# Optimization experiments

Measured on AMD Instinct MI355X. Metric: run time of the kernel, lower is better.

## Reference

```python
import jax, jax.numpy as jnp
import numpy as np

B, N, C_IN, C_OUT, H_MLP, STEPS, DEG = 8, 128, 512, 512, 128, 10, 16
E = B * N * DEG  # edges per side


def _seg_mean(v, idx, n):
    s = jax.ops.segment_sum(v, idx, num_segments=n)
    c = jax.ops.segment_sum(jnp.ones((v.shape[0], 1), v.dtype), idx, num_segments=n)
    return s / jnp.maximum(c, 1.0)


def _relconv(x, ei, W1, W2, Wr, br):
    n = x.shape[0]
    src, dst = ei[0], ei[1]
    out1 = _seg_mean((x @ W1)[src], dst, n)  # flow source_to_target, mean aggr
    out2 = _seg_mean((x @ W2)[dst], src, n)  # flow target_to_source, mean aggr
    return x @ Wr + br + out1 + out2


def _gnn(x, ei, p):
    # GNNForEmbedding: 1 RelConv layer, LayerNorm(relu(.)), cat=True, lin=True (eval: dropout off)
    W1, W2, Wr, br, g, b, Fw, Fb = p
    h = jax.nn.relu(_relconv(x, ei, W1, W2, Wr, br))
    mu = h.mean(-1, keepdims=True)
    var = ((h - mu) ** 2).mean(-1, keepdims=True)
    h = (h - mu) / jnp.sqrt(var + 1e-5) * g + b
    return jnp.concatenate([x, h], -1) @ Fw + Fb


def setup_inputs():
    key = jax.random.key(0)
    ks = jax.random.split(key, 20)
    nn_ = B * N

    def randn(k, shape, s=1.0):
        return jax.random.normal(k, shape, jnp.float32) * s

    def mk_edges(k):
        k1, k2 = jax.random.split(k)
        off = jnp.repeat(jnp.arange(B, dtype=jnp.int32) * N, N * DEG)
        src = jax.random.randint(k1, (E,), 0, N, jnp.int32) + off
        dst = jax.random.randint(k2, (E,), 0, N, jnp.int32) + off
        return jnp.stack([src, dst])

    s = 0.04
    inp = {
        'x_s': randn(ks[0], (nn_, C_IN)),
        'edge_index_s': mk_edges(ks[1]),
        'edge_attr_s': randn(ks[2], (E, 1)),
        'batch_s': jnp.repeat(jnp.arange(B, dtype=jnp.int32), N),
        'x_t': randn(ks[3], (nn_, C_IN)),
        'edge_index_t': mk_edges(ks[4]),
        'edge_attr_t': randn(ks[5], (E, 1)),
        'batch_t': jnp.repeat(jnp.arange(B, dtype=jnp.int32), N),
        'e_lin1': randn(ks[6], (C_IN, C_OUT), s),
        'e_lin2': randn(ks[7], (C_IN, C_OUT), s),
        'e_rw': randn(ks[8], (C_IN, C_OUT), s),
        'e_rb': jnp.zeros((C_OUT,), jnp.float32),
        'e_g': jnp.ones((C_OUT,), jnp.float32),
        'e_b': jnp.zeros((C_OUT,), jnp.float32),
        'e_fw': randn(ks[9], (C_IN + C_OUT, C_OUT), s),
        'e_fb': jnp.zeros((C_OUT,), jnp.float32),
        'c_lin1': randn(ks[10], (C_IN, C_OUT), s),
        'c_lin2': randn(ks[11], (C_IN, C_OUT), s),
        'c_rw': randn(ks[12], (C_IN, C_OUT), s),
        'c_rb': jnp.zeros((C_OUT,), jnp.float32),
        'c_g': jnp.ones((C_OUT,), jnp.float32),
        'c_b': jnp.zeros((C_OUT,), jnp.float32),
        'c_fw': randn(ks[13], (C_IN + C_OUT, C_OUT), s),
        'c_fb': jnp.zeros((C_OUT,), jnp.float32),
        'm_w1': randn(ks[14], (C_OUT, H_MLP), s),
        'm_b1': jnp.zeros((H_MLP,), jnp.float32),
        'm_w2': randn(ks[15], (H_MLP,), s),
        'm_b2': jnp.zeros((), jnp.float32),
    }
    return inp


def reference(x_s, edge_index_s, edge_attr_s, batch_s, x_t, edge_index_t, edge_attr_t, batch_t,
              e_lin1, e_lin2, e_rw, e_rb, e_g, e_b, e_fw, e_fb,
              c_lin1, c_lin2, c_rw, c_rb, c_g, c_b, c_fw, c_fb,
              m_w1, m_b1, m_w2, m_b2):
    pe = (e_lin1, e_lin2, e_rw, e_rb, e_g, e_b, e_fw, e_fb)
    pc = (c_lin1, c_lin2, c_rw, c_rb, c_g, c_b, c_fw, c_fb)
    # embedding GNN (detached in original model)
    Hs = jax.lax.stop_gradient(_gnn(x_s, edge_index_s, pe)).reshape(B, N, C_OUT)
    Ht = jax.lax.stop_gradient(_gnn(x_t, edge_index_t, pe)).reshape(B, N, C_OUT)
    # all graphs have exactly N nodes -> masks are all-True, masked_softmax == softmax
    S_hat = jnp.einsum('bsc,btc->bst', Hs, Ht)
    S_0 = jax.nn.softmax(S_hat, axis=-1).reshape(B * N, N)
    rkey = jax.random.key(42)
    for t in range(STEPS):
        S = jax.nn.softmax(S_hat, axis=-1)
        R_s = jax.random.normal(jax.random.fold_in(rkey, t), (B, N, C_IN), jnp.float32)
        R_t = jnp.einsum('bst,bsc->btc', S, R_s)  # S^T @ R_s
        O_s = _gnn(R_s.reshape(-1, C_IN), edge_index_s, pc).reshape(B, N, C_OUT)
        O_t = _gnn(R_t.reshape(-1, C_IN), edge_index_t, pc).reshape(B, N, C_OUT)
        # fc1(O_s_i - O_t_j) = O_s_i@W1 - O_t_j@W1 + b1 (linearity): avoid O(Ns*Nt*C) diff tensor
        A = O_s @ m_w1 + m_b1          # [B, Ns, H]
        Bm = O_t @ m_w1                # [B, Nt, H]
        hid = jax.nn.relu(A[:, :, None, :] - Bm[:, None, :, :])  # [B, Ns, Nt, H]
        S_hat = S_hat + (hid @ m_w2 + m_b2)
    S_L = jax.nn.softmax(S_hat, axis=-1).reshape(B * N, N)
    return (S_0, S_L)
```

## Files before the change

kernel.cpp:

```cpp
#include <hip/hip_runtime.h>
#include <stdint.h>


typedef unsigned short u16;
typedef unsigned int u32;
typedef __attribute__((ext_vector_type(8))) short short8;
typedef __attribute__((ext_vector_type(4))) float f32x4;

__device__ inline u16 f2bf(float x) {
  u32 u = __float_as_uint(x);
  u32 r = (u + 0x7fffu + ((u >> 16) & 1u)) >> 16;
  return (u16)r;
}
__device__ inline float bf2f(u16 h) { return __uint_as_float(((u32)h) << 16); }
__device__ inline void split2(float x, u16& h, u16& l) {
  h = f2bf(x);
  l = f2bf(x - bf2f(h));
}

__host__ __device__ inline void tf2x32(uint32_t k0, uint32_t k1, uint32_t x0,
                                       uint32_t x1, uint32_t& o0, uint32_t& o1) {
  uint32_t ks0 = k0, ks1 = k1, ks2 = 0x1BD11BDAu ^ k0 ^ k1;
  x0 += ks0; x1 += ks1;
#define TF_R(r) { x0 += x1; x1 = (x1 << r) | (x1 >> (32 - r)); x1 ^= x0; }
  TF_R(13) TF_R(15) TF_R(26) TF_R(6)   x0 += ks1; x1 += ks2 + 1u;
  TF_R(17) TF_R(29) TF_R(16) TF_R(24)  x0 += ks2; x1 += ks0 + 2u;
  TF_R(13) TF_R(15) TF_R(26) TF_R(6)   x0 += ks0; x1 += ks1 + 3u;
  TF_R(17) TF_R(29) TF_R(16) TF_R(24)  x0 += ks1; x1 += ks2 + 4u;
  TF_R(13) TF_R(15) TF_R(26) TF_R(6)   x0 += ks2; x1 += ks0 + 5u;
#undef TF_R
  o0 = x0; o1 = x1;
}

__device__ inline float erfinv_f(float x) {
  float w = -log1pf(-x * x);
  float p;
  if (w < 5.0f) {
    w = w - 2.5f;
    p = 2.81022636e-08f;
    p = fmaf(p, w, 3.43273939e-07f);
    p = fmaf(p, w, -3.5233877e-06f);
    p = fmaf(p, w, -4.39150654e-06f);
    p = fmaf(p, w, 0.00021858087f);
    p = fmaf(p, w, -0.00125372503f);
    p = fmaf(p, w, -0.00417768164f);
    p = fmaf(p, w, 0.246640727f);
    p = fmaf(p, w, 1.50140941f);
  } else {
    w = sqrtf(w) - 3.0f;
    p = -0.000200214257f;
    p = fmaf(p, w, 0.000100950558f);
    p = fmaf(p, w, 0.00134934322f);
    p = fmaf(p, w, -0.00367342844f);
    p = fmaf(p, w, 0.00573950773f);
    p = fmaf(p, w, -0.0076224613f);
    p = fmaf(p, w, 0.00943887047f);
    p = fmaf(p, w, 1.00167406f);
    p = fmaf(p, w, 2.83297682f);
  }
  return p * x;
}

__device__ inline float bits_to_normal(uint32_t bits) {
  uint32_t fb = (bits >> 9) | 0x3f800000u;
  float f = __uint_as_float(fb) - 1.0f;
  float u = f * 2.0f + (-0.99999994f);
  u = fmaxf(-0.99999994f, u);
  return 1.41421356f * erfinv_f(u);
}

template <int OUTP, int BIASN, int BIASM, int AGGB>
__global__ __launch_bounds__(256) void mfma_gemm(
    int K,
    const u16* __restrict__ Ah, const u16* __restrict__ Al, int lda, int sA,
    const u16* __restrict__ Bh, const u16* __restrict__ Bl, int ldb, int sB,
    float* __restrict__ Cf, u16* __restrict__ Ch, u16* __restrict__ Cl,
    int ldc, int sC, const float* __restrict__ bias) {
  const int g = blockIdx.z;
  Ah += (size_t)g * sA; Al += (size_t)g * sA;
  Bh += (size_t)g * sB; Bl += (size_t)g * sB;
  if (OUTP) { Ch += (size_t)g * sC; Cl += (size_t)g * sC; }
  else { Cf += (size_t)g * sC; }
  __shared__ u16 As[2][64][64];
  __shared__ u16 Bs[2][64][64];
  const int tid = threadIdx.x;
  const int m0 = blockIdx.y * 64, n0 = blockIdx.x * 64;
  const int l = tid & 63;
  const int w = tid >> 6;
  const int wr = (w >> 1) * 32, wc = (w & 1) * 32;
  const int l15 = l & 15, lq = l >> 4;
  f32x4 acc[2][2] = {};
  const int sr = tid >> 3, sc = tid & 7;
  for (int k0 = 0; k0 < K; k0 += 64) {
    __syncthreads();
#pragma unroll
    for (int p = 0; p < 2; ++p) {
      int r = sr + p * 32;
      int dst = (sc ^ (r & 7)) * 8;
      *(uint4*)&As[0][r][dst] = *(const uint4*)&Ah[(size_t)(m0 + r) * lda + k0 + sc * 8];
      *(uint4*)&As[1][r][dst] = *(const uint4*)&Al[(size_t)(m0 + r) * lda + k0 + sc * 8];
      size_t boff;
      if (AGGB) {
        int rowg = (k0 < 128) ? (n0 + r) : (512 + n0 + r);
        boff = (size_t)rowg * ldb + (k0 & 127) + sc * 8;
      } else {
        boff = (size_t)(n0 + r) * ldb + k0 + sc * 8;
      }
      *(uint4*)&Bs[0][r][dst] = *(const uint4*)&Bh[boff];
      *(uint4*)&Bs[1][r][dst] = *(const uint4*)&Bl[boff];
    }
    __syncthreads();
#pragma unroll
    for (int kk = 0; kk < 2; ++kk) {
      short8 aH[2], aL[2], bH[2], bL[2];
#pragma unroll
      for (int i = 0; i < 2; ++i) {
        int mr = wr + i * 16 + l15;
        int ca = ((kk * 4 + lq) ^ (mr & 7)) * 8;
        aH[i] = *(const short8*)&As[0][mr][ca];
        aL[i] = *(const short8*)&As[1][mr][ca];
        int nr = wc + i * 16 + l15;
        int cb = ((kk * 4 + lq) ^ (nr & 7)) * 8;
        bH[i] = *(const short8*)&Bs[0][nr][cb];
        bL[i] = *(const short8*)&Bs[1][nr][cb];
      }
#pragma unroll
      for (int i = 0; i < 2; ++i)
#pragma unroll
        for (int j = 0; j < 2; ++j) {
          acc[i][j] = __builtin_amdgcn_mfma_f32_16x16x32_bf16(aH[i], bH[j], acc[i][j], 0, 0, 0);
          acc[i][j] = __builtin_amdgcn_mfma_f32_16x16x32_bf16(aL[i], bH[j], acc[i][j], 0, 0, 0);
          acc[i][j] = __builtin_amdgcn_mfma_f32_16x16x32_bf16(aH[i], bL[j], acc[i][j], 0, 0, 0);
        }
    }
  }
#pragma unroll
  for (int i = 0; i < 2; ++i)
#pragma unroll
    for (int j = 0; j < 2; ++j) {
      int n = n0 + wc + j * 16 + l15;
      int mb = m0 + wr + i * 16 + lq * 4;
      f32x4 v = acc[i][j];
      if (BIASN) {
        float b = bias[n];
        v[0] += b; v[1] += b; v[2] += b; v[3] += b;
      }
      if (BIASM) {
        f32x4 bb = *(const f32x4*)&bias[mb];
        v[0] += bb[0]; v[1] += bb[1]; v[2] += bb[2]; v[3] += bb[3];
      }
      if (OUTP) {
        u16 h[4], lo[4];
        split2(v[0], h[0], lo[0]); split2(v[1], h[1], lo[1]);
        split2(v[2], h[2], lo[2]); split2(v[3], h[3], lo[3]);
        uint2 hv = {(u32)h[0] | ((u32)h[1] << 16), (u32)h[2] | ((u32)h[3] << 16)};
        uint2 lv = {(u32)lo[0] | ((u32)lo[1] << 16), (u32)lo[2] | ((u32)lo[3] << 16)};
        *(uint2*)&Ch[(size_t)n * ldc + mb] = hv;
        *(uint2*)&Cl[(size_t)n * ldc + mb] = lv;
      } else {
        *(f32x4*)&Cf[(size_t)n * ldc + mb] = v;
      }
    }
}

template <int BIASM>
__global__ __launch_bounds__(512) void mfma_gemm_big(
    int K,
    const u16* __restrict__ Ah, const u16* __restrict__ Al, int lda,
    const u16* __restrict__ Bh, const u16* __restrict__ Bl, int ldb,
    u16* __restrict__ Ch, u16* __restrict__ Cl, int ldc,
    const float* __restrict__ bias) {
  __shared__ u16 As[2][128][64];
  __shared__ u16 Bs[2][128][64];
  const int tid = threadIdx.x;
  const int m0 = blockIdx.y * 128, n0 = blockIdx.x * 128;
  const int l = tid & 63;
  const int w = tid >> 6;
  const int wm = (w >> 2) * 64;
  const int wn = (w & 3) * 32;
  const int l15 = l & 15, lq = l >> 4;
  f32x4 acc[4][2] = {};
  const int sr = tid >> 3, sc = tid & 7;
  for (int k0 = 0; k0 < K; k0 += 64) {
    __syncthreads();
#pragma unroll
    for (int p = 0; p < 2; ++p) {
      int r = p * 64 + sr;
      int dst = (sc ^ (r & 7)) * 8;
      *(uint4*)&As[0][r][dst] = *(const uint4*)&Ah[(size_t)(m0 + r) * lda + k0 + sc * 8];
      *(uint4*)&As[1][r][dst] = *(const uint4*)&Al[(size_t)(m0 + r) * lda + k0 + sc * 8];
      *(uint4*)&Bs[0][r][dst] = *(const uint4*)&Bh[(size_t)(n0 + r) * ldb + k0 + sc * 8];
      *(uint4*)&Bs[1][r][dst] = *(const uint4*)&Bl[(size_t)(n0 + r) * ldb + k0 + sc * 8];
    }
    __syncthreads();
#pragma unroll
    for (int kk = 0; kk < 2; ++kk) {
      short8 aH[4], aL[4], bH[2], bL[2];
#pragma unroll
      for (int i = 0; i < 4; ++i) {
        int mr = wm + i * 16 + l15;
        int ca = ((kk * 4 + lq) ^ (mr & 7)) * 8;
        aH[i] = *(const short8*)&As[0][mr][ca];
        aL[i] = *(const short8*)&As[1][mr][ca];
      }
#pragma unroll
      for (int j = 0; j < 2; ++j) {
        int nr = wn + j * 16 + l15;
        int cb = ((kk * 4 + lq) ^ (nr & 7)) * 8;
        bH[j] = *(const short8*)&Bs[0][nr][cb];
        bL[j] = *(const short8*)&Bs[1][nr][cb];
      }
#pragma unroll
      for (int i = 0; i < 4; ++i)
#pragma unroll
        for (int j = 0; j < 2; ++j) {
          acc[i][j] = __builtin_amdgcn_mfma_f32_16x16x32_bf16(aH[i], bH[j], acc[i][j], 0, 0, 0);
          acc[i][j] = __builtin_amdgcn_mfma_f32_16x16x32_bf16(aL[i], bH[j], acc[i][j], 0, 0, 0);
          acc[i][j] = __builtin_amdgcn_mfma_f32_16x16x32_bf16(aH[i], bL[j], acc[i][j], 0, 0, 0);
        }
    }
  }
#pragma unroll
  for (int i = 0; i < 4; ++i)
#pragma unroll
    for (int j = 0; j < 2; ++j) {
      int n = n0 + wn + j * 16 + l15;
      int mb = m0 + wm + i * 16 + lq * 4;
      f32x4 v = acc[i][j];
      if (BIASM) {
        f32x4 bb = *(const f32x4*)&bias[mb];
        v[0] += bb[0]; v[1] += bb[1]; v[2] += bb[2]; v[3] += bb[3];
      }
      u16 h[4], lo[4];
      split2(v[0], h[0], lo[0]); split2(v[1], h[1], lo[1]);
      split2(v[2], h[2], lo[2]); split2(v[3], h[3], lo[3]);
      uint2 hv = {(u32)h[0] | ((u32)h[1] << 16), (u32)h[2] | ((u32)h[3] << 16)};
      uint2 lv = {(u32)lo[0] | ((u32)lo[1] << 16), (u32)lo[2] | ((u32)lo[3] << 16)};
      *(uint2*)&Ch[(size_t)n * ldc + mb] = hv;
      *(uint2*)&Cl[(size_t)n * ldc + mb] = lv;
    }
}

__global__ __launch_bounds__(256) void count_kernel(const int* __restrict__ ei_s,
                                                    const int* __restrict__ ei_t,
                                                    int* __restrict__ Acnt,
                                                    int* __restrict__ degd,
                                                    int* __restrict__ degs) {
  int e = blockIdx.x * 256 + threadIdx.x;
  int side = e >> 14, idx = e & 16383;
  const int* ei = side ? ei_t : ei_s;
  int src = ei[idx], dst = ei[16384 + idx];
  int g = (dst >> 7) + side * 8;
  int dl = dst & 127, sl = src & 127;
  atomicAdd(&Acnt[(g * 128 + dl) * 128 + sl], 1);
  atomicAdd(&degd[g * 128 + dl], 1);
  atomicAdd(&degs[g * 128 + sl], 1);
}

__global__ __launch_bounds__(256) void norm_adj_kernel(const int* __restrict__ Acnt,
                                                       const int* __restrict__ degd,
                                                       const int* __restrict__ degs,
                                                       u16* __restrict__ Mh,
                                                       u16* __restrict__ Ml) {
  int idx = blockIdx.x * 256 + threadIdx.x;
  int g = idx >> 15, m = (idx >> 8) & 127, k = idx & 255;
  float val;
  if (k < 128)
    val = (float)Acnt[(g * 128 + m) * 128 + k] / (float)max(degd[g * 128 + m], 1);
  else
    val = (float)Acnt[(g * 128 + (k - 128)) * 128 + m] / (float)max(degs[g * 128 + m], 1);
  u16 h, lo;
  split2(val, h, lo);
  Mh[idx] = h; Ml[idx] = lo;
}

__global__ __launch_bounds__(256) void pack_kernel(const float* __restrict__ W1,
                                                   const float* __restrict__ W2,
                                                   const float* __restrict__ Wr,
                                                   float* __restrict__ Wcat) {
  int idx = blockIdx.x * 256 + threadIdx.x;
  int k = idx / 384, j4 = (idx % 384) * 4;
  float4 v;
  if (j4 < 512)       v = *(const float4*)&W1[k * 512 + j4];
  else if (j4 < 1024) v = *(const float4*)&W2[k * 512 + j4 - 512];
  else                v = *(const float4*)&Wr[k * 512 + j4 - 1024];
  *(float4*)&Wcat[k * 1536 + j4] = v;
}

__global__ __launch_bounds__(256) void convert_wT(const float* __restrict__ W,
                                                  u16* __restrict__ Th,
                                                  u16* __restrict__ Tl,
                                                  int K, int N) {
  int id = blockIdx.x * 256 + threadIdx.x;
  int k = id / N, n = id - k * N;
  u16 h, lo;
  split2(W[id], h, lo);
  Th[n * K + k] = h;
  Tl[n * K + k] = lo;
}

__global__ __launch_bounds__(128) void fbm_kernel(const float* __restrict__ fb,
                                                  const float* __restrict__ w1,
                                                  const float* __restrict__ b1,
                                                  float* __restrict__ fbm) {
  int h = threadIdx.x;
  float acc = b1[h];
  for (int c = 0; c < 512; ++c) acc = fmaf(fb[c], w1[c * 128 + h], acc);
  fbm[h] = acc;
}

__global__ __launch_bounds__(256) void copyx_kernel(const float* __restrict__ xs,
                                                    const float* __restrict__ xt,
                                                    u16* __restrict__ XHh,
                                                    u16* __restrict__ XHl) {
  int idx = blockIdx.x * 256 + threadIdx.x;
  int row = idx >> 7, c4 = (idx & 127) << 2;
  const float* src = (row < 1024) ? (xs + row * 512 + c4)
                                  : (xt + (row - 1024) * 512 + c4);
  float4 v = *(const float4*)src;
  u16 h[4], lo[4];
  split2(v.x, h[0], lo[0]); split2(v.y, h[1], lo[1]);
  split2(v.z, h[2], lo[2]); split2(v.w, h[3], lo[3]);
  uint2 hv = {(u32)h[0] | ((u32)h[1] << 16), (u32)h[2] | ((u32)h[3] << 16)};
  uint2 lv = {(u32)lo[0] | ((u32)lo[1] << 16), (u32)lo[2] | ((u32)lo[3] << 16)};
  *(uint2*)&XHh[row * 1024 + c4] = hv;
  *(uint2*)&XHl[row * 1024 + c4] = lv;
}

__global__ __launch_bounds__(256) void gemm_f32(
    int M, int N, int K,
    const float* __restrict__ A, int lda,
    const float* __restrict__ B, int ldb,
    float* __restrict__ C, int ldc) {
  int m0 = blockIdx.y * 64, n0 = blockIdx.x * 64;
  __shared__ float As[16][64];
  __shared__ float Bs[16][64];
  int tid = threadIdx.x;
  int tx = tid & 15, ty = tid >> 4;
  float acc[4][4] = {};
  for (int k0 = 0; k0 < K; k0 += 16) {
    {
      int m_l = tid & 63, k_l = (tid >> 6) << 2;
      float4 av = *(const float4*)&A[(m0 + m_l) * lda + k0 + k_l];
      As[k_l + 0][m_l] = av.x; As[k_l + 1][m_l] = av.y;
      As[k_l + 2][m_l] = av.z; As[k_l + 3][m_l] = av.w;
    }
    {
      int k_l = tid >> 4, n_l = (tid & 15) << 2;
      float4 bv = *(const float4*)&B[(k0 + k_l) * ldb + n0 + n_l];
      *(float4*)&Bs[k_l][n_l] = bv;
    }
    __syncthreads();
#pragma unroll
    for (int kk = 0; kk < 16; ++kk) {
      float4 a4 = *(const float4*)&As[kk][ty << 2];
      float4 b4 = *(const float4*)&Bs[kk][tx << 2];
      float av[4] = {a4.x, a4.y, a4.z, a4.w};
      float bv[4] = {b4.x, b4.y, b4.z, b4.w};
#pragma unroll
      for (int i = 0; i < 4; ++i)
#pragma unroll
        for (int j = 0; j < 4; ++j) acc[i][j] = fmaf(av[i], bv[j], acc[i][j]);
    }
    __syncthreads();
  }
#pragma unroll
  for (int i = 0; i < 4; ++i) {
    int m = m0 + (ty << 2) + i;
    float4 v = {acc[i][0], acc[i][1], acc[i][2], acc[i][3]};
    *(float4*)&C[m * ldc + n0 + (tx << 2)] = v;
  }
}

__global__ __launch_bounds__(256) void ln_stats(
    const u16* __restrict__ Yth, const u16* __restrict__ Ytl,
    const float* __restrict__ AGGt, const float* __restrict__ rb,
    float* __restrict__ partS, float* __restrict__ partQ) {
  int cg = blockIdx.x, ng = blockIdx.y;
  int lane = threadIdx.x & 63, cs = threadIdx.x >> 6;
  int node = ng * 64 + lane;
  float s = 0.f, q = 0.f;
#pragma unroll
  for (int k = 0; k < 16; ++k) {
    int c = cg * 64 + cs * 16 + k;
    size_t yi = (size_t)(1024 + c) * 2048 + node;
    float v = bf2f(Yth[yi]) + bf2f(Ytl[yi]) + rb[c] + AGGt[(size_t)c * 2048 + node];
    v = fmaxf(v, 0.f);
    s += v; q += v * v;
  }
  __shared__ float ls[4][64], lq[4][64];
  ls[cs][lane] = s; lq[cs][lane] = q;
  __syncthreads();
  if (cs == 0) {
    s = ls[0][lane] + ls[1][lane] + ls[2][lane] + ls[3][lane];
    q = lq[0][lane] + lq[1][lane] + lq[2][lane] + lq[3][lane];
    partS[cg * 2048 + node] = s;
    partQ[cg * 2048 + node] = q;
  }
}

__global__ __launch_bounds__(256) void ln_apply(
    const u16* __restrict__ Yth, const u16* __restrict__ Ytl,
    const float* __restrict__ AGGt, const float* __restrict__ partS,
    const float* __restrict__ partQ, const float* __restrict__ rb,
    const float* __restrict__ gam, const float* __restrict__ bet,
    u16* __restrict__ XHh, u16* __restrict__ XHl) {
  int cg = blockIdx.x, ng = blockIdx.y;
  int lane = threadIdx.x & 63, cs = threadIdx.x >> 6;
  int node = ng * 64 + lane;
  float s = 0.f, q = 0.f;
#pragma unroll
  for (int p = 0; p < 8; ++p) {
    s += partS[p * 2048 + node];
    q += partQ[p * 2048 + node];
  }
  float mu = s * (1.f / 512.f);
  float var = q * (1.f / 512.f) - mu * mu;
  float inv = 1.f / sqrtf(var + 1e-5f);
  __shared__ u16 oth[64][66], otl[64][66];
#pragma unroll
  for (int k = 0; k < 16; ++k) {
    int c = cg * 64 + cs * 16 + k;
    size_t yi = (size_t)(1024 + c) * 2048 + node;
    float v = bf2f(Yth[yi]) + bf2f(Ytl[yi]) + rb[c] + AGGt[(size_t)c * 2048 + node];
    v = fmaxf(v, 0.f);
    float o = (v - mu) * inv * gam[c] + bet[c];
    u16 h, lo;
    split2(o, h, lo);
    oth[lane][cs * 16 + k] = h;
    otl[lane][cs * 16 + k] = lo;
  }
  __syncthreads();
  int nl = threadIdx.x >> 2, cq = (threadIdx.x & 3) * 16;
  size_t xbase = (size_t)(ng * 64 + nl) * 1024 + 512 + cg * 64 + cq;
  uint4 h0, h1, l0, l1;
  h0 = *(const uint4*)&oth[nl][cq];     h1 = *(const uint4*)&oth[nl][cq + 8];
  l0 = *(const uint4*)&otl[nl][cq];     l1 = *(const uint4*)&otl[nl][cq + 8];
  *(uint4*)&XHh[xbase] = h0;  *(uint4*)&XHh[xbase + 8] = h1;
  *(uint4*)&XHl[xbase] = l0;  *(uint4*)&XHl[xbase + 8] = l1;
}

__global__ __launch_bounds__(256) void tail_kernel(
    float* __restrict__ SH, const float* __restrict__ Pt,
    const float* __restrict__ b1, const float* __restrict__ w2,
    const float* __restrict__ b2,
    u16* __restrict__ STh, u16* __restrict__ STl,
    u16* __restrict__ RsTh, u16* __restrict__ RsTl,
    u16* __restrict__ XHh, u16* __restrict__ XHl,
    float* __restrict__ outp, int do_rng, u32 k0, u32 k1) {
  int bid = blockIdx.x;
  int tid = threadIdx.x;
  if (bid < 512) {
    int rl = tid >> 7;
    int t = tid & 127;
    int bs = bid * 2 + rl;
    int gg = bs >> 7, s = bs & 127;
    float val = SH[bs * 128 + t];
    if (Pt) {
      __shared__ float arow[2][128], w2s[128];
      arow[rl][t] = Pt[(size_t)t * 2048 + bs] + b1[t];
      if (tid < 128) w2s[tid] = w2[tid];
      __syncthreads();
      const float* pt = Pt + 1024 + gg * 128 + t;
      float acc = 0.f;
#pragma unroll 8
      for (int h = 0; h < 128; ++h) {
        float pv = pt[(size_t)h * 2048];
        acc += fmaxf(arow[rl][h] - pv, 0.f) * w2s[h];
      }
      val += acc + b2[0];
      SH[bs * 128 + t] = val;
    }
    float m = val;
#pragma unroll
    for (int off = 32; off > 0; off >>= 1) m = fmaxf(m, __shfl_xor(m, off));
    __shared__ float redm[4], reds[4];
    int wv = tid >> 6;
    if ((tid & 63) == 0) redm[wv] = m;
    __syncthreads();
    m = fmaxf(redm[wv], redm[wv ^ 1]);
    float e = expf(val - m);
    float su = e;
#pragma unroll
    for (int off = 32; off > 0; off >>= 1) su += __shfl_xor(su, off);
    if ((tid & 63) == 0) reds[wv] = su;
    __syncthreads();
    su = reds[wv] + reds[wv ^ 1];
    float p = e / su;
    u16 h, lo;
    split2(p, h, lo);
    STh[(gg * 128 + t) * 128 + s] = h;
    STl[(gg * 128 + t) * 128 + s] = lo;
    if (outp) outp[bs * 128 + t] = p;
  } else if (do_rng) {
    u32 j = (u32)(bid - 512) * 256 + tid;
    u32 o0, o1;
    tf2x32(k0, k1, 0u, j, o0, o1);
    float val = bits_to_normal(o0 ^ o1);
    u32 node = j >> 9, ch = j & 511;
    u16 h, lo;
    split2(val, h, lo);
    XHh[node * 1024 + ch] = h;
    XHl[node * 1024 + ch] = lo;
    RsTh[ch * 1024 + node] = h;
    RsTl[ch * 1024 + node] = lo;
  }
}

extern "C" void kernel_launch(void* const* d_in, const int* in_sizes, int n_in,
                              void* d_out, int out_size, void* d_ws, size_t ws_size,
                              hipStream_t stream) {
  const float* x_s = (const float*)d_in[0];
  const int* ei_s = (const int*)d_in[1];
  const float* x_t = (const float*)d_in[4];
  const int* ei_t = (const int*)d_in[5];
  const float* e_lin1 = (const float*)d_in[8];
  const float* e_lin2 = (const float*)d_in[9];
  const float* e_rw = (const float*)d_in[10];
  const float* e_rb = (const float*)d_in[11];
  const float* e_g = (const float*)d_in[12];
  const float* e_b = (const float*)d_in[13];
  const float* e_fw = (const float*)d_in[14];
  const float* e_fb = (const float*)d_in[15];
  const float* c_lin1 = (const float*)d_in[16];
  const float* c_lin2 = (const float*)d_in[17];
  const float* c_rw = (const float*)d_in[18];
  const float* c_rb = (const float*)d_in[19];
  const float* c_g = (const float*)d_in[20];
  const float* c_b = (const float*)d_in[21];
  const float* c_fw = (const float*)d_in[22];
  const float* c_fb = (const float*)d_in[23];
  const float* m_w1 = (const float*)d_in[24];
  const float* m_b1 = (const float*)d_in[25];
  const float* m_w2 = (const float*)d_in[26];
  const float* m_b2 = (const float*)d_in[27];
  float* out = (float*)d_out;
  float* ws = (float*)d_ws;

  u16* Mch   = (u16*)(ws + 0);
  u16* Mcl   = (u16*)(ws + 262144);
  u16* Yth   = (u16*)(ws + 524288);
  u16* Ytl   = (u16*)(ws + 2097152);
  float* AGGt = ws + 3670016;
  float* Pt   = AGGt;
  u16* XHh   = (u16*)(ws + 4718592);
  u16* XHl   = (u16*)(ws + 5767168);
  u16* WTeh  = (u16*)(ws + 6815744);
  u16* WTel  = (u16*)(ws + 7208960);
  u16* WTch  = (u16*)(ws + 7602176);
  u16* WTcl  = (u16*)(ws + 7995392);
  u16* FTeh  = (u16*)(ws + 8388608);
  u16* FTel  = (u16*)(ws + 8650752);
  u16* FmTh  = (u16*)(ws + 8912896);
  u16* FmTl  = (u16*)(ws + 8978432);
  u16* Oh    = (u16*)(ws + 9043968);
  u16* Ol    = (u16*)(ws + 9568256);
  u16* RsTh  = (u16*)(ws + 10092544);
  u16* RsTl  = (u16*)(ws + 10354688);
  u16* STh   = (u16*)(ws + 10616832);
  u16* STl   = (u16*)(ws + 10682368);
  float* SH  = ws + 10747904;
  float* Wstage = ws + 10878976;
  float* fbm = ws + 11665408;
  float* partS = ws + 11665536;
  float* partQ = ws + 11681920;
  int* Acnt  = (int*)Yth;
  int* degd  = Acnt + 262144;
  int* degs  = degd + 2048;

  hipMemsetAsync(Acnt, 0, (262144 + 4096) * sizeof(int), stream);
  count_kernel<<<128, 256, 0, stream>>>(ei_s, ei_t, Acnt, degd, degs);
  norm_adj_kernel<<<2048, 256, 0, stream>>>(Acnt, degd, degs, Mch, Mcl);
  pack_kernel<<<768, 256, 0, stream>>>(e_lin1, e_lin2, e_rw, Wstage);
  convert_wT<<<3072, 256, 0, stream>>>(Wstage, WTeh, WTel, 512, 1536);
  pack_kernel<<<768, 256, 0, stream>>>(c_lin1, c_lin2, c_rw, Wstage);
  convert_wT<<<3072, 256, 0, stream>>>(Wstage, WTch, WTcl, 512, 1536);
  convert_wT<<<2048, 256, 0, stream>>>(e_fw, FTeh, FTel, 1024, 512);
  gemm_f32<<<dim3(2, 16, 1), 256, 0, stream>>>(1024, 128, 512, c_fw, 512,
                                               m_w1, 128, Wstage, 128);
  convert_wT<<<512, 256, 0, stream>>>(Wstage, FmTh, FmTl, 1024, 128);
  fbm_kernel<<<1, 128, 0, stream>>>(c_fb, m_w1, m_b1, fbm);
  copyx_kernel<<<1024, 256, 0, stream>>>(x_s, x_t, XHh, XHl);

  auto relu_ln = [&](const float* rb, const float* g, const float* bb) {
    ln_stats<<<dim3(8, 32), 256, 0, stream>>>(Yth, Ytl, AGGt, rb, partS, partQ);
    ln_apply<<<dim3(8, 32), 256, 0, stream>>>(Yth, Ytl, AGGt, partS, partQ,
                                              rb, g, bb, XHh, XHl);
  };

  mfma_gemm_big<0><<<dim3(12, 16), 512, 0, stream>>>(
      512, XHh, XHl, 1024, WTeh, WTel, 512, Yth, Ytl, 2048, nullptr);
  mfma_gemm<0, 0, 0, 1><<<dim3(8, 2, 16), 256, 0, stream>>>(
      256, Mch, Mcl, 256, 32768, Yth, Ytl, 2048, 128,
      AGGt, nullptr, nullptr, 2048, 128, nullptr);
  relu_ln(e_rb, e_g, e_b);
  mfma_gemm_big<1><<<dim3(16, 4), 512, 0, stream>>>(
      1024, FTeh, FTel, 1024, XHh, XHl, 1024, Oh, Ol, 512, e_fb);
  mfma_gemm<0, 0, 0, 0><<<dim3(2, 2, 8), 256, 0, stream>>>(
      512, Oh + 1024 * 512, Ol + 1024 * 512, 512, 128 * 512,
      Oh, Ol, 512, 128 * 512,
      SH, nullptr, nullptr, 128, 16384, nullptr);

  {
    uint32_t fk0, fk1;
    tf2x32(0u, 42u, 0u, 0u, fk0, fk1);
    tail_kernel<<<2560, 256, 0, stream>>>(SH, nullptr, m_b1, m_w2, m_b2,
                                          STh, STl, RsTh, RsTl, XHh, XHl,
                                          out, 1, fk0, fk1);
  }

  for (int t = 0; t < 10; ++t) {
    mfma_gemm<1, 0, 0, 0><<<dim3(2, 8, 8), 256, 0, stream>>>(
        128, RsTh, RsTl, 1024, 128, STh, STl, 128, 16384,
        nullptr, XHh + 1024 * 1024, XHl + 1024 * 1024, 1024, 128 * 1024, nullptr);
    mfma_gemm_big<0><<<dim3(12, 16), 512, 0, stream>>>(
        512, XHh, XHl, 1024, WTch, WTcl, 512, Yth, Ytl, 2048, nullptr);
    mfma_gemm<0, 0, 0, 1><<<dim3(8, 2, 16), 256, 0, stream>>>(
        256, Mch, Mcl, 256, 32768, Yth, Ytl, 2048, 128,
        AGGt, nullptr, nullptr, 2048, 128, nullptr);
    relu_ln(c_rb, c_g, c_b);
    mfma_gemm<0, 1, 0, 0><<<dim3(2, 32, 1), 256, 0, stream>>>(
        1024, XHh, XHl, 1024, 0, FmTh, FmTl, 1024, 0,
        Pt, nullptr, nullptr, 2048, 0, fbm);
    uint32_t fk0, fk1;
    tf2x32(0u, 42u, 0u, (uint32_t)(t + 1), fk0, fk1);
    int do_rng = (t < 9) ? 1 : 0;
    tail_kernel<<<do_rng ? 2560 : 512, 256, 0, stream>>>(
        SH, Pt, m_b1, m_w2, m_b2, STh, STl, RsTh, RsTl, XHh, XHl,
        (t == 9) ? (out + 131072) : nullptr, do_rng, fk0, fk1);
  }
}
```

Baseline: 1.040 ms.

## Fuse ReLU and LayerNorm stats into aggregation GEMM, split-K the Pt GEMM

The aggregation GEMM epilogue now adds the root term and bias, applies ReLU, writes the activated result, and accumulates per-node sum and sum-of-squares through LDS and global atomics. This removes the separate ln_stats kernel and the re-read of Y in ln_apply. The Pt projection GEMM is split four ways along K and reduces with float atomics into a buffer that the preceding big GEMM zeroes, which gives the GPU more blocks. Weight packing and conversion are merged into one kernel. In exchange, atomics make the float summation order nondeterministic, and the zeroing work adds extra stores to the big GEMM.

Measured after the change: 1.112 ms. +6.9%, slower.

```diff
diff --git a/kernel.cpp b/kernel.cpp
--- a/kernel.cpp
+++ b/kernel.cpp
@@ -69,13 +69,16 @@
   return 1.41421356f * erfinv_f(u);
 }
 
-template <int OUTP, int BIASN, int BIASM, int AGGB>
+template <int OUTP, int BIASN, int BIASM, int AGGB, int RELULN, int ATOMIC>
 __global__ __launch_bounds__(256) void mfma_gemm(
     int K,
     const u16* __restrict__ Ah, const u16* __restrict__ Al, int lda, int sA,
     const u16* __restrict__ Bh, const u16* __restrict__ Bl, int ldb, int sB,
     float* __restrict__ Cf, u16* __restrict__ Ch, u16* __restrict__ Cl,
-    int ldc, int sC, const float* __restrict__ bias) {
+    int ldc, int sC, const float* __restrict__ bias,
+    const u16* __restrict__ Y2h, const u16* __restrict__ Y2l,
+    const float* __restrict__ rb2, float* __restrict__ pS,
+    float* __restrict__ pQ) {
   const int g = blockIdx.z;
   Ah += (size_t)g * sA; Al += (size_t)g * sA;
   Bh += (size_t)g * sB; Bl += (size_t)g * sB;
@@ -83,6 +86,7 @@
   else { Cf += (size_t)g * sC; }
   __shared__ u16 As[2][64][64];
   __shared__ u16 Bs[2][64][64];
+  __shared__ float s_lds[64], q_lds[64];
   const int tid = threadIdx.x;
   const int m0 = blockIdx.y * 64, n0 = blockIdx.x * 64;
   const int l = tid & 63;
@@ -91,6 +95,7 @@
   const int l15 = l & 15, lq = l >> 4;
   f32x4 acc[2][2] = {};
   const int sr = tid >> 3, sc = tid & 7;
+  if (RELULN && tid < 64) { s_lds[tid] = 0.f; q_lds[tid] = 0.f; }
   for (int k0 = 0; k0 < K; k0 += 64) {
     __syncthreads();
 #pragma unroll
@@ -134,6 +139,7 @@
         }
     }
   }
+  float sv[2][4] = {}, qv[2][4] = {};
 #pragma unroll
   for (int i = 0; i < 2; ++i)
 #pragma unroll
@@ -141,15 +147,34 @@
       int n = n0 + wc + j * 16 + l15;
       int mb = m0 + wr + i * 16 + lq * 4;
       f32x4 v = acc[i][j];
-      if (BIASN) {
+      if (BIASN && (!ATOMIC || g == 0)) {
         float b = bias[n];
         v[0] += b; v[1] += b; v[2] += b; v[3] += b;
       }
-      if (BIASM) {
+      if (BIASM && (!ATOMIC || g == 0)) {
         f32x4 bb = *(const f32x4*)&bias[mb];
         v[0] += bb[0]; v[1] += bb[1]; v[2] += bb[2]; v[3] += bb[3];
       }
-      if (OUTP) {
+      if (RELULN) {
+        int gm = g * 128 + mb;
+        float rbn = rb2[n];
+        uint2 yh = *(const uint2*)&Y2h[(size_t)(1024 + n) * 2048 + gm];
+        uint2 yl = *(const uint2*)&Y2l[(size_t)(1024 + n) * 2048 + gm];
+        v[0] = fmaxf(v[0] + bf2f((u16)(yh.x & 0xffff)) + bf2f((u16)(yl.x & 0xffff)) + rbn, 0.f);
+        v[1] = fmaxf(v[1] + bf2f((u16)(yh.x >> 16)) + bf2f((u16)(yl.x >> 16)) + rbn, 0.f);
+        v[2] = fmaxf(v[2] + bf2f((u16)(yh.y & 0xffff)) + bf2f((u16)(yl.y & 0xffff)) + rbn, 0.f);
+        v[3] = fmaxf(v[3] + bf2f((u16)(yh.y >> 16)) + bf2f((u16)(yl.y >> 16)) + rbn, 0.f);
+#pragma unroll
+        for (int r = 0; r < 4; ++r) {
+          sv[i][r] += v[r];
+          qv[i][r] += v[r] * v[r];
+        }
+        *(f32x4*)&Cf[(size_t)n * ldc + mb] = v;
+      } else if (ATOMIC) {
+#pragma unroll
+        for (int r = 0; r < 4; ++r)
+          atomicAdd(&Cf[(size_t)n * ldc + mb + r], v[r]);
+      } else if (OUTP) {
         u16 h[4], lo[4];
         split2(v[0], h[0], lo[0]); split2(v[1], h[1], lo[1]);
         split2(v[2], h[2], lo[2]); split2(v[3], h[3], lo[3]);
@@ -161,6 +186,21 @@
         *(f32x4*)&Cf[(size_t)n * ldc + mb] = v;
       }
     }
+  if (RELULN) {
+#pragma unroll
+    for (int i = 0; i < 2; ++i)
+#pragma unroll
+      for (int r = 0; r < 4; ++r) {
+        int nl = wr + i * 16 + lq * 4 + r;
+        atomicAdd(&s_lds[nl], sv[i][r]);
+        atomicAdd(&q_lds[nl], qv[i][r]);
+      }
+    __syncthreads();
+    if (tid < 64) {
+      atomicAdd(&pS[g * 128 + m0 + tid], s_lds[tid]);
+      atomicAdd(&pQ[g * 128 + m0 + tid], q_lds[tid]);
+    }
+  }
 }
 
 template <int BIASM>
@@ -169,10 +209,19 @@
     const u16* __restrict__ Ah, const u16* __restrict__ Al, int lda,
     const u16* __restrict__ Bh, const u16* __restrict__ Bl, int ldb,
     u16* __restrict__ Ch, u16* __restrict__ Cl, int ldc,
-    const float* __restrict__ bias) {
+    const float* __restrict__ bias, float* __restrict__ pS,
+    float* __restrict__ pQ, float* __restrict__ Ptz) {
   __shared__ u16 As[2][128][64];
   __shared__ u16 Bs[2][128][64];
   const int tid = threadIdx.x;
+  const int bid = blockIdx.y * gridDim.x + blockIdx.x;
+  const int nb = gridDim.x * gridDim.y;
+  if (bid == 0) {
+    for (int i = tid; i < 2048; i += 512) { pS[i] = 0.f; pQ[i] = 0.f; }
+  }
+  float4 z4 = {0.f, 0.f, 0.f, 0.f};
+  for (int i = bid * 512 + tid; i < 65536; i += nb * 512)
+    ((float4*)Ptz)[i] = z4;
   const int m0 = blockIdx.y * 128, n0 = blockIdx.x * 128;
   const int l = tid & 63;
   const int w = tid >> 6;
@@ -274,17 +323,18 @@
   Mh[idx] = h; Ml[idx] = lo;
 }
 
-__global__ __launch_bounds__(256) void pack_kernel(const float* __restrict__ W1,
-                                                   const float* __restrict__ W2,
-                                                   const float* __restrict__ Wr,
-                                                   float* __restrict__ Wcat) {
-  int idx = blockIdx.x * 256 + threadIdx.x;
-  int k = idx / 384, j4 = (idx % 384) * 4;
-  float4 v;
-  if (j4 < 512)       v = *(const float4*)&W1[k * 512 + j4];
-  else if (j4 < 1024) v = *(const float4*)&W2[k * 512 + j4 - 512];
-  else                v = *(const float4*)&Wr[k * 512 + j4 - 1024];
-  *(float4*)&Wcat[k * 1536 + j4] = v;
+__global__ __launch_bounds__(256) void convert_packed(const float* __restrict__ W1,
+                                                      const float* __restrict__ W2,
+                                                      const float* __restrict__ Wr,
+                                                      u16* __restrict__ Th,
+                                                      u16* __restrict__ Tl) {
+  int id = blockIdx.x * 256 + threadIdx.x;
+  int n = id >> 9, k = id & 511;
+  const float* W = (n < 512) ? W1 : ((n < 1024) ? W2 : Wr);
+  float v = W[k * 512 + (n & 511)];
+  u16 h, lo;
+  split2(v, h, lo);
+  Th[id] = h; Tl[id] = lo;
 }
 
 __global__ __launch_bounds__(256) void convert_wT(const float* __restrict__ W,
@@ -372,48 +422,15 @@
   }
 }
 
-__global__ __launch_bounds__(256) void ln_stats(
-    const u16* __restrict__ Yth, const u16* __restrict__ Ytl,
-    const float* __restrict__ AGGt, const float* __restrict__ rb,
-    float* __restrict__ partS, float* __restrict__ partQ) {
+__global__ __launch_bounds__(256) void ln_apply(
+    const float* __restrict__ AGGt, const float* __restrict__ pS,
+    const float* __restrict__ pQ, const float* __restrict__ gam,
+    const float* __restrict__ bet, u16* __restrict__ XHh,
+    u16* __restrict__ XHl) {
   int cg = blockIdx.x, ng = blockIdx.y;
   int lane = threadIdx.x & 63, cs = threadIdx.x >> 6;
   int node = ng * 64 + lane;
-  float s = 0.f, q = 0.f;
-#pragma unroll
-  for (int k = 0; k < 16; ++k) {
-    int c = cg * 64 + cs * 16 + k;
-    size_t yi = (size_t)(1024 + c) * 2048 + node;
-    float v = bf2f(Yth[yi]) + bf2f(Ytl[yi]) + rb[c] + AGGt[(size_t)c * 2048 + node];
-    v = fmaxf(v, 0.f);
-    s += v; q += v * v;
-  }
-  __shared__ float ls[4][64], lq[4][64];
-  ls[cs][lane] = s; lq[cs][lane] = q;
-  __syncthreads();
-  if (cs == 0) {
-    s = ls[0][lane] + ls[1][lane] + ls[2][lane] + ls[3][lane];
-    q = lq[0][lane] + lq[1][lane] + lq[2][lane] + lq[3][lane];
-    partS[cg * 2048 + node] = s;
-    partQ[cg * 2048 + node] = q;
-  }
-}
-
-__global__ __launch_bounds__(256) void ln_apply(
-    const u16* __restrict__ Yth, const u16* __restrict__ Ytl,
-    const float* __restrict__ AGGt, const float* __restrict__ partS,
-    const float* __restrict__ partQ, const float* __restrict__ rb,
-    const float* __restrict__ gam, const float* __restrict__ bet,
-    u16* __restrict__ XHh, u16* __restrict__ XHl) {
-  int cg = blockIdx.x, ng = blockIdx.y;
-  int lane = threadIdx.x & 63, cs = threadIdx.x >> 6;
-  int node = ng * 64 + lane;
-  float s = 0.f, q = 0.f;
-#pragma unroll
-  for (int p = 0; p < 8; ++p) {
-    s += partS[p * 2048 + node];
-    q += partQ[p * 2048 + node];
-  }
+  float s = pS[node], q = pQ[node];
   float mu = s * (1.f / 512.f);
   float var = q * (1.f / 512.f) - mu * mu;
   float inv = 1.f / sqrtf(var + 1e-5f);
@@ -421,9 +438,7 @@
 #pragma unroll
   for (int k = 0; k < 16; ++k) {
     int c = cg * 64 + cs * 16 + k;
-    size_t yi = (size_t)(1024 + c) * 2048 + node;
-    float v = bf2f(Yth[yi]) + bf2f(Ytl[yi]) + rb[c] + AGGt[(size_t)c * 2048 + node];
-    v = fmaxf(v, 0.f);
+    float v = AGGt[(size_t)c * 2048 + node];
     float o = (v - mu) * inv * gam[c] + bet[c];
     u16 h, lo;
     split2(o, h, lo);
@@ -542,7 +557,6 @@
   u16* Yth   = (u16*)(ws + 524288);
   u16* Ytl   = (u16*)(ws + 2097152);
   float* AGGt = ws + 3670016;
-  float* Pt   = AGGt;
   u16* XHh   = (u16*)(ws + 4718592);
   u16* XHl   = (u16*)(ws + 5767168);
   u16* WTeh  = (u16*)(ws + 6815744);
@@ -561,9 +575,10 @@
   u16* STl   = (u16*)(ws + 10682368);
   float* SH  = ws + 10747904;
   float* Wstage = ws + 10878976;
+  float* Pt  = ws + 11010048;
   float* fbm = ws + 11665408;
   float* partS = ws + 11665536;
-  float* partQ = ws + 11681920;
+  float* partQ = ws + 11667584;
   int* Acnt  = (int*)Yth;
   int* degd  = Acnt + 262144;
   int* degs  = degd + 2048;
@@ -571,10 +586,8 @@
   hipMemsetAsync(Acnt, 0, (262144 + 4096) * sizeof(int), stream);
   count_kernel<<<128, 256, 0, stream>>>(ei_s, ei_t, Acnt, degd, degs);
   norm_adj_kernel<<<2048, 256, 0, stream>>>(Acnt, degd, degs, Mch, Mcl);
-  pack_kernel<<<768, 256, 0, stream>>>(e_lin1, e_lin2, e_rw, Wstage);
-  convert_wT<<<3072, 256, 0, stream>>>(Wstage, WTeh, WTel, 512, 1536);
-  pack_kernel<<<768, 256, 0, stream>>>(c_lin1, c_lin2, c_rw, Wstage);
-  convert_wT<<<3072, 256, 0, stream>>>(Wstage, WTch, WTcl, 512, 1536);
+  convert_packed<<<3072, 256, 0, stream>>>(e_lin1, e_lin2, e_rw, WTeh, WTel);
+  convert_packed<<<3072, 256, 0, stream>>>(c_lin1, c_lin2, c_rw, WTch, WTcl);
   convert_wT<<<2048, 256, 0, stream>>>(e_fw, FTeh, FTel, 1024, 512);
   gemm_f32<<<dim3(2, 16, 1), 256, 0, stream>>>(1024, 128, 512, c_fw, 512,
                                                m_w1, 128, Wstage, 128);
@@ -582,24 +595,23 @@
   fbm_kernel<<<1, 128, 0, stream>>>(c_fb, m_w1, m_b1, fbm);
   copyx_kernel<<<1024, 256, 0, stream>>>(x_s, x_t, XHh, XHl);
 
-  auto relu_ln = [&](const float* rb, const float* g, const float* bb) {
-    ln_stats<<<dim3(8, 32), 256, 0, stream>>>(Yth, Ytl, AGGt, rb, partS, partQ);
-    ln_apply<<<dim3(8, 32), 256, 0, stream>>>(Yth, Ytl, AGGt, partS, partQ,
-                                              rb, g, bb, XHh, XHl);
-  };
-
   mfma_gemm_big<0><<<dim3(12, 16), 512, 0, stream>>>(
-      512, XHh, XHl, 1024, WTeh, WTel, 512, Yth, Ytl, 2048, nullptr);
-  mfma_gemm<0, 0, 0, 1><<<dim3(8, 2, 16), 256, 0, stream>>>(
+      512, XHh, XHl, 1024, WTeh, WTel, 512, Yth, Ytl, 2048, nullptr,
+      partS, partQ, Pt);
+  mfma_gemm<0, 0, 0, 1, 1, 0><<<dim3(8, 2, 16), 256, 0, stream>>>(
       256, Mch, Mcl, 256, 32768, Yth, Ytl, 2048, 128,
-      AGGt, nullptr, nullptr, 2048, 128, nullptr);
-  relu_ln(e_rb, e_g, e_b);
+      AGGt, nullptr, nullptr, 2048, 128, nullptr,
+      Yth, Ytl, e_rb, partS, partQ);
+  ln_apply<<<dim3(8, 32), 256, 0, stream>>>(AGGt, partS, partQ, e_g, e_b,
+                                            XHh, XHl);
   mfma_gemm_big<1><<<dim3(16, 4), 512, 0, stream>>>(
-      1024, FTeh, FTel, 1024, XHh, XHl, 1024, Oh, Ol, 512, e_fb);
-  mfma_gemm<0, 0, 0, 0><<<dim3(2, 2, 8), 256, 0, stream>>>(
+      1024, FTeh, FTel, 1024, XHh, XHl, 1024, Oh, Ol, 512, e_fb,
+      partS, partQ, Pt);
+  mfma_gemm<0, 0, 0, 0, 0, 0><<<dim3(2, 2, 8), 256, 0, stream>>>(
       512, Oh + 1024 * 512, Ol + 1024 * 512, 512, 128 * 512,
       Oh, Ol, 512, 128 * 512,
-      SH, nullptr, nullptr, 128, 16384, nullptr);
+      SH, nullptr, nullptr, 128, 16384, nullptr,
+      nullptr, nullptr, nullptr, nullptr, nullptr);
 
   {
     uint32_t fk0, fk1;
@@ -610,18 +622,23 @@
   }
 
   for (int t = 0; t < 10; ++t) {
-    mfma_gemm<1, 0, 0, 0><<<dim3(2, 8, 8), 256, 0, stream>>>(
+    mfma_gemm<1, 0, 0, 0, 0, 0><<<dim3(2, 8, 8), 256, 0, stream>>>(
         128, RsTh, RsTl, 1024, 128, STh, STl, 128, 16384,
-        nullptr, XHh + 1024 * 1024, XHl + 1024 * 1024, 1024, 128 * 1024, nullptr);
+        nullptr, XHh + 1024 * 1024, XHl + 1024 * 1024, 1024, 128 * 1024, nullptr,
+        nullptr, nullptr, nullptr, nullptr, nullptr);
     mfma_gemm_big<0><<<dim3(12, 16), 512, 0, stream>>>(
-        512, XHh, XHl, 1024, WTch, WTcl, 512, Yth, Ytl, 2048, nullptr);
-    mfma_gemm<0, 0, 0, 1><<<dim3(8, 2, 16), 256, 0, stream>>>(
+        512, XHh, XHl, 1024, WTch, WTcl, 512, Yth, Ytl, 2048, nullptr,
+        partS, partQ, Pt);
+    mfma_gemm<0, 0, 0, 1, 1, 0><<<dim3(8, 2, 16), 256, 0, stream>>>(
         256, Mch, Mcl, 256, 32768, Yth, Ytl, 2048, 128,
-        AGGt, nullptr, nullptr, 2048, 128, nullptr);
-    relu_ln(c_rb, c_g, c_b);
-    mfma_gemm<0, 1, 0, 0><<<dim3(2, 32, 1), 256, 0, stream>>>(
-        1024, XHh, XHl, 1024, 0, FmTh, FmTl, 1024, 0,
-        Pt, nullptr, nullptr, 2048, 0, fbm);
+        AGGt, nullptr, nullptr, 2048, 128, nullptr,
+        Yth, Ytl, c_rb, partS, partQ);
+    ln_apply<<<dim3(8, 32), 256, 0, stream>>>(AGGt, partS, partQ, c_g, c_b,
+                                              XHh, XHl);
+    mfma_gemm<0, 1, 0, 0, 0, 1><<<dim3(2, 32, 4), 256, 0, stream>>>(
+        256, XHh, XHl, 1024, 256, FmTh, FmTl, 1024, 256,
+        Pt, nullptr, nullptr, 2048, 0, fbm,
+        nullptr, nullptr, nullptr, nullptr, nullptr);
     uint32_t fk0, fk1;
     tf2x32(0u, 42u, 0u, (uint32_t)(t + 1), fk0, fk1);
     int do_rng = (t < 9) ? 1 : 0;
```
